# Optimization experiments

Measured on AMD Instinct MI355X. Metric: run time of the kernel, lower is better.

Reference implementation:

```python
import jax, jax.numpy as jnp
import numpy as np

N_NODES = 100000


def gcn_conv(x, src, dst, W, b):
    """PyG GCNConv: add self-loops, symmetric D^-1/2 (A+I) D^-1/2 normalization.
    x: [N, Fin]; src/dst: [E'] (self-loops already appended); W: [Fin, Fout]; b: [Fout].
    """
    xw = x @ W  # [N, Fout]
    ones = jnp.ones(dst.shape[0], dtype=x.dtype)
    deg = jax.ops.segment_sum(ones, dst, num_segments=N_NODES)  # in-degree incl. self-loop
    dinv = jnp.where(deg > 0, jax.lax.rsqrt(deg), 0.0)
    norm = dinv[src] * dinv[dst]  # [E']
    msg = xw[src] * norm[:, None]  # gather + scale
    out = jax.ops.segment_sum(msg, dst, num_segments=N_NODES)  # scatter-add
    return out + b


def setup_inputs() -> dict:
    key = jax.random.key(0)
    ks = jax.random.split(key, 12)
    hidden = 64
    E = 1600000
    x_node = jax.random.normal(ks[0], (N_NODES, 1), dtype=jnp.float32)
    edge_index = jax.random.randint(ks[1], (2, E), 0, N_NODES, dtype=jnp.int64)

    def glorot(k, fan_in, fan_out):
        lim = float(np.sqrt(6.0 / (fan_in + fan_out)))
        return jax.random.uniform(k, (fan_in, fan_out), jnp.float32, -lim, lim)

    W1 = glorot(ks[2], 1, hidden)
    b1 = jnp.zeros((hidden,), jnp.float32)
    W2 = glorot(ks[3], hidden, hidden)
    b2 = jnp.zeros((hidden,), jnp.float32)
    W3 = glorot(ks[4], hidden, hidden)
    b3 = jnp.zeros((hidden,), jnp.float32)
    W4 = glorot(ks[5], hidden, 1)
    b4 = jnp.zeros((1,), jnp.float32)
    return {"x_node": x_node, "edge_index": edge_index,
            "W1": W1, "b1": b1, "W2": W2, "b2": b2,
            "W3": W3, "b3": b3, "W4": W4, "b4": b4}


def reference(x_node, edge_index, W1, b1, W2, b2, W3, b3, W4, b4):
    # Append self-loops once (shared by both GCN layers, as PyG does per-layer with identical result)
    loops = jnp.arange(N_NODES, dtype=edge_index.dtype)
    src = jnp.concatenate([edge_index[0], loops])
    dst = jnp.concatenate([edge_index[1], loops])

    h = jax.nn.silu(gcn_conv(x_node, src, dst, W1, b1))
    h = jax.nn.silu(gcn_conv(h, src, dst, W2, b2))
    h = jax.nn.silu(h @ W3 + b3)
    return h @ W4 + b4  # [N, 1]
```

## Files before the change

### kernel.cpp

```cpp
#include <hip/hip_runtime.h>
#include <math.h>

#define N_NODES 100000
#define NPB    196
#define NBUCK  511
#define CAP    3584
#define CHUNKA 2048

#define NCHEB  15
#define SMAX   8.0f

__device__ __forceinline__ float silu_f(float x) {
    return x * __builtin_amdgcn_rcpf(1.0f + __builtin_amdgcn_exp2f(-1.442695041f * x));
}

__device__ __forceinline__ float bcast_f(float v, int lane) {
    return __int_as_float(__builtin_amdgcn_readlane(__float_as_int(v), lane));
}

__global__ __launch_bounds__(64) void k_cheb(const float* __restrict__ W1,
                                             const float* __restrict__ b1,
                                             float* __restrict__ cheb) {
    int f = threadIdx.x;
    float w = W1[f], b = b1[f];
    float g[NCHEB], th[NCHEB];
    const float pi = 3.14159265358979f;
#pragma unroll
    for (int j = 0; j < NCHEB; ++j) {
        th[j] = (j + 0.5f) * (pi / NCHEB);
        float S = SMAX * __cosf(th[j]);
        float y = fmaf(w, S, b);
        g[j] = y / (1.0f + expf(-y));
    }
#pragma unroll
    for (int k = 0; k < NCHEB; ++k) {
        float s = 0.f;
#pragma unroll
        for (int j = 0; j < NCHEB; ++j)
            s += g[j] * __cosf((float)k * th[j]);
        cheb[k * 64 + f] = s * ((k == 0) ? (1.0f / NCHEB) : (2.0f / NCHEB));
    }
}

__global__ __launch_bounds__(512) void k_bucket(const int* __restrict__ src,
                                                const int* __restrict__ dst,
                                                int* __restrict__ gcur,
                                                unsigned int* __restrict__ buf, int E) {
    __shared__ unsigned hist[512];
    __shared__ unsigned lbase[512];
    __shared__ unsigned gbase[512];
    __shared__ unsigned lcur[512];
    __shared__ unsigned wtot[8];
    __shared__ unsigned pay[CHUNKA];
    __shared__ unsigned short bkt[CHUNKA];
    int t = threadIdx.x;
    int lane = t & 63, wid = t >> 6;
    hist[t] = 0;
    __syncthreads();
    int e0 = blockIdx.x * CHUNKA;
    int e1 = min(e0 + CHUNKA, E);
    for (int e = e0 + t; e < e1; e += 512)
        atomicAdd(&hist[dst[e] / NPB], 1u);
    __syncthreads();
    unsigned v = hist[t], sc = v;
#pragma unroll
    for (int off = 1; off < 64; off <<= 1) {
        unsigned y = __shfl_up(sc, off, 64);
        if (lane >= off) sc += y;
    }
    if (lane == 63) wtot[wid] = sc;
    __syncthreads();
    unsigned add = 0;
    for (int w = 0; w < wid; ++w) add += wtot[w];
    unsigned ex = sc - v + add;
    lbase[t] = ex;
    gbase[t] = v ? (unsigned)atomicAdd(&gcur[t], (int)v) : 0u;
    lcur[t] = 0;
    __syncthreads();
    for (int e = e0 + t; e < e1; e += 512) {
        int d = dst[e];
        int s = src[e];
        int b = d / NPB;
        unsigned pos = lbase[b] + atomicAdd(&lcur[b], 1u);
        pay[pos] = ((unsigned)s << 8) | (unsigned)(d - b * NPB);
        bkt[pos] = (unsigned short)b;
    }
    __syncthreads();
    int cb = e1 - e0;
    for (int i = t; i < cb; i += 512) {
        int b = bkt[i];
        unsigned gp = gbase[b] + ((unsigned)i - lbase[b]);
        if (gp < CAP)
            buf[(size_t)b * CAP + gp] = pay[i];
    }
}

__global__ __launch_bounds__(512) void k_build(const int* __restrict__ gcur,
                                               unsigned int* __restrict__ buf,
                                               const float* __restrict__ x,
                                               int* __restrict__ rowptr,
                                               int* __restrict__ cnt,
                                               float* __restrict__ dinv,
                                               float* __restrict__ xs, int N) {
    __shared__ unsigned hist[256];
    __shared__ unsigned cur[256];
    __shared__ unsigned wtot[4];
    __shared__ unsigned lsrc[CAP];
    int b = blockIdx.x;
    int t = threadIdx.x;
    int lane = t & 63, wid = t >> 6;
    int cb = min(gcur[b], CAP);
    int n0 = b * NPB;
    int np = min(N - n0, NPB);
    unsigned int* bb = buf + (size_t)b * CAP;

    if (t < 256) hist[t] = 0;
    __syncthreads();
    for (int i = t; i < cb; i += 512) atomicAdd(&hist[bb[i] & 255u], 1u);
    __syncthreads();
    unsigned v = (t < 256) ? hist[t] : 0u, sc = v;
#pragma unroll
    for (int off = 1; off < 64; off <<= 1) {
        unsigned y = __shfl_up(sc, off, 64);
        if (lane >= off) sc += y;
    }
    if (lane == 63 && t < 256) wtot[wid] = sc;
    __syncthreads();
    unsigned add = 0;
    for (int w = 0; w < wid && w < 4; ++w) add += wtot[w];
    unsigned ex = sc - v + add;
    if (t < 256) cur[t] = ex;
    if (t < np) {
        int node = n0 + t;
        int deg = (int)v;
        cnt[node] = deg;
        rowptr[node] = b * CAP + (int)ex;
        float dv = rsqrtf((float)(deg + 1));
        dinv[node] = dv;
        xs[node] = x[node] * dv;
    }
    __syncthreads();
    for (int i = t; i < cb; i += 512) {
        unsigned p = bb[i];
        unsigned pos = atomicAdd(&cur[p & 255u], 1u);
        lsrc[pos] = p >> 8;
    }
    __syncthreads();
    for (int i = t; i < cb; i += 512) bb[i] = lsrc[i];
}

__global__ __launch_bounds__(256) void k_sd(const int* __restrict__ rowptr,
                                            const int* __restrict__ cnt,
                                            const int* __restrict__ csr,
                                            const float* __restrict__ xs,
                                            const float* __restrict__ dinv,
                                            float2* __restrict__ sd, int N) {
    int t = blockIdx.x * 256 + threadIdx.x;
    int i = t >> 3, sub = t & 7;
    if (i >= N) return;
    int start = rowptr[i], deg = cnt[i];
    float sum = 0.f;
    int ia = (sub < deg) ? csr[start + sub] : -1;
    int ib = (sub + 8 < deg) ? csr[start + sub + 8] : -1;
    if (ia >= 0) sum += xs[ia];
    if (ib >= 0) sum += xs[ib];
    for (int j = sub + 16; j < deg; j += 8) sum += xs[csr[start + j]];
    sum += __shfl_xor(sum, 1, 64);
    sum += __shfl_xor(sum, 2, 64);
    sum += __shfl_xor(sum, 4, 64);
    if (sub == 0) {
        float d = dinv[i];
        sd[i] = make_float2((sum + xs[i]) * d, d);
    }
}

__global__ __launch_bounds__(256, 8) void k_final(
    const int* __restrict__ rowptr, const int* __restrict__ cnt,
    const int* __restrict__ csr, const float2* __restrict__ sd,
    const float* __restrict__ cheb,
    const float* __restrict__ W2, const float* __restrict__ b2,
    const float* __restrict__ W3, const float* __restrict__ b3,
    const float* __restrict__ W4, const float* __restrict__ b4,
    float* __restrict__ out, int N)
{
    __shared__ float sA[64 * 65];
    __shared__ float sP[4 * 64];

    const int lane = threadIdx.x & 63;
    const int wid  = __builtin_amdgcn_readfirstlane(threadIdx.x >> 6);
    const int tile0 = blockIdx.x * 64;
    const int nbase = tile0 + wid * 16;
    const int row0  = wid * 16;

    const int nloc = lane >> 2, sub = lane & 3;
    const int i = nbase + nloc;
    const bool valid = (i < N);
    int start = 0, deg = 0;
    float2 self = make_float2(0.f, 0.f);
    if (valid) {
        start = rowptr[i];
        deg   = cnt[i];
        self  = sd[i];
    }

    float m[NCHEB];
    {
        float d = (sub == 0) ? self.y : 0.f;
        float t = fminf(fmaxf(self.x * (1.0f / SMAX), -1.f), 1.f);
        float t2 = t + t, Tm = 1.f, Tc = t;
        m[0] = d;
        m[1] = d * t;
#pragma unroll
        for (int k = 2; k < NCHEB; ++k) {
            float Tn = fmaf(t2, Tc, -Tm);
            m[k] = d * Tn;
            Tm = Tc; Tc = Tn;
        }
    }
    for (int j = sub; j < deg; j += 4) {
        int u = csr[start + j];
        float2 su = sd[u];
        float d = su.y;
        float t = fminf(fmaxf(su.x * (1.0f / SMAX), -1.f), 1.f);
        float t2 = t + t, Tm = 1.f, Tc = t;
        m[0] += d;
        m[1] = fmaf(d, t, m[1]);
#pragma unroll
        for (int k = 2; k < NCHEB; ++k) {
            float Tn = fmaf(t2, Tc, -Tm);
            m[k] = fmaf(d, Tn, m[k]);
            Tm = Tc; Tc = Tn;
        }
    }
#pragma unroll
    for (int k = 0; k < NCHEB; ++k) {
        m[k] += __shfl_xor(m[k], 1, 64);
        m[k] += __shfl_xor(m[k], 2, 64);
    }

    float ck[NCHEB];
#pragma unroll
    for (int k = 0; k < NCHEB; ++k) ck[k] = cheb[k * 64 + lane];
#pragma unroll
    for (int nl = 0; nl < 16; ++nl) {
        float acc = 0.f;
#pragma unroll
        for (int k = 0; k < NCHEB; ++k)
            acc = fmaf(ck[k], bcast_f(m[k], 4 * nl), acc);
        float dv = bcast_f(self.y, 4 * nl);
        sA[(row0 + nl) * 65 + lane] = acc * dv;
    }
    __syncthreads();

    const int f0 = wid * 16;
    float acc2[16];
#pragma unroll
    for (int j = 0; j < 16; ++j) acc2[j] = b2[f0 + j];
    for (int k = 0; k < 64; ++k) {
        float av = sA[lane * 65 + k];
#pragma unroll
        for (int j = 0; j < 16; ++j)
            acc2[j] = fmaf(av, W2[k * 64 + f0 + j], acc2[j]);
    }
    __syncthreads();
#pragma unroll
    for (int j = 0; j < 16; ++j)
        sA[lane * 65 + f0 + j] = silu_f(acc2[j]);
    __syncthreads();

    float acc3[16];
#pragma unroll
    for (int j = 0; j < 16; ++j) acc3[j] = b3[f0 + j];
    for (int k = 0; k < 64; ++k) {
        float uv = sA[lane * 65 + k];
#pragma unroll
        for (int j = 0; j < 16; ++j)
            acc3[j] = fmaf(uv, W3[k * 64 + f0 + j], acc3[j]);
    }
    float part = 0.f;
#pragma unroll
    for (int j = 0; j < 16; ++j)
        part = fmaf(silu_f(acc3[j]), W4[f0 + j], part);
    sP[wid * 64 + lane] = part;
    __syncthreads();

    if (wid == 0) {
        int i2 = tile0 + lane;
        if (i2 < N)
            out[i2] = sP[lane] + sP[64 + lane] + sP[128 + lane] + sP[192 + lane] + b4[0];
    }
}

extern "C" void kernel_launch(void* const* d_in, const int* in_sizes, int n_in,
                              void* d_out, int out_size, void* d_ws, size_t ws_size,
                              hipStream_t stream) {
    const float* x  = (const float*)d_in[0];
    const int* edge = (const int*)d_in[1];
    const float* W1 = (const float*)d_in[2];
    const float* b1 = (const float*)d_in[3];
    const float* W2 = (const float*)d_in[4];
    const float* b2 = (const float*)d_in[5];
    const float* W3 = (const float*)d_in[6];
    const float* b3 = (const float*)d_in[7];
    const float* W4 = (const float*)d_in[8];
    const float* b4 = (const float*)d_in[9];
    float* out = (float*)d_out;

    const int N = N_NODES;
    const int E = in_sizes[1] / 2;
    const int* src = edge;
    const int* dst = edge + E;
    const int NCHUNK = (E + CHUNKA - 1) / CHUNKA;

    char* ws = (char*)d_ws;
    size_t off = 0;
    int*    gcur   = (int*)(ws + off);    off += 512 * 4;
    float2* sd     = (float2*)(ws + off); off += (size_t)N * 8;
    int*    rowptr = (int*)(ws + off);    off += (size_t)N * 4;
    int*    cnt    = (int*)(ws + off);    off += (size_t)N * 4;
    float*  dinv   = (float*)(ws + off);  off += (size_t)N * 4;
    float*  xs     = (float*)(ws + off);  off += (size_t)N * 4;
    float*  cheb   = (float*)(ws + off);  off += NCHEB * 64 * 4;
    unsigned int* buf = (unsigned int*)(ws + off); off += (size_t)NBUCK * CAP * 4;
    int* csr = (int*)buf;

    hipMemsetAsync(gcur, 0, 512 * 4, stream);

    k_cheb  <<<1, 64, 0, stream>>>(W1, b1, cheb);
    k_bucket<<<NCHUNK, 512, 0, stream>>>(src, dst, gcur, buf, E);
    k_build <<<NBUCK, 512, 0, stream>>>(gcur, buf, x, rowptr, cnt, dinv, xs, N);
    k_sd    <<<(N * 8 + 255) / 256, 256, 0, stream>>>(rowptr, cnt, csr, xs, dinv, sd, N);
    k_final <<<(N + 63) / 64, 256, 0, stream>>>(rowptr, cnt, csr, sd, cheb,
                                                W2, b2, W3, b3, W4, b4, out, N);
}
```

Before: 165.8 us.

## Replace bucketed CSR build with atomic degree count, global scan and scatter

```diff
diff --git a/kernel.cpp b/kernel.cpp
--- a/kernel.cpp
+++ b/kernel.cpp
@@ -2,13 +2,9 @@
 #include <math.h>
 
 #define N_NODES 100000
-#define NPB    196
-#define NBUCK  511
-#define CAP    3584
-#define CHUNKA 2048
-
 #define NCHEB  15
 #define SMAX   8.0f
+#define SCAN_B 391
 
 __device__ __forceinline__ float silu_f(float x) {
     return x * __builtin_amdgcn_rcpf(1.0f + __builtin_amdgcn_exp2f(-1.442695041f * x));
@@ -18,159 +14,116 @@
     return __int_as_float(__builtin_amdgcn_readlane(__float_as_int(v), lane));
 }
 
-__global__ __launch_bounds__(64) void k_cheb(const float* __restrict__ W1,
+__global__ __launch_bounds__(256) void k_deg(const int* __restrict__ dst,
+                                             int* __restrict__ cnt,
+                                             const float* __restrict__ W1,
                                              const float* __restrict__ b1,
-                                             float* __restrict__ cheb) {
-    int f = threadIdx.x;
-    float w = W1[f], b = b1[f];
-    float g[NCHEB], th[NCHEB];
-    const float pi = 3.14159265358979f;
-#pragma unroll
-    for (int j = 0; j < NCHEB; ++j) {
-        th[j] = (j + 0.5f) * (pi / NCHEB);
-        float S = SMAX * __cosf(th[j]);
-        float y = fmaf(w, S, b);
-        g[j] = y / (1.0f + expf(-y));
-    }
-#pragma unroll
-    for (int k = 0; k < NCHEB; ++k) {
-        float s = 0.f;
-#pragma unroll
-        for (int j = 0; j < NCHEB; ++j)
-            s += g[j] * __cosf((float)k * th[j]);
-        cheb[k * 64 + f] = s * ((k == 0) ? (1.0f / NCHEB) : (2.0f / NCHEB));
-    }
-}
-
-__global__ __launch_bounds__(512) void k_bucket(const int* __restrict__ src,
-                                                const int* __restrict__ dst,
-                                                int* __restrict__ gcur,
-                                                unsigned int* __restrict__ buf, int E) {
-    __shared__ unsigned hist[512];
-    __shared__ unsigned lbase[512];
-    __shared__ unsigned gbase[512];
-    __shared__ unsigned lcur[512];
-    __shared__ unsigned wtot[8];
-    __shared__ unsigned pay[CHUNKA];
-    __shared__ unsigned short bkt[CHUNKA];
-    int t = threadIdx.x;
-    int lane = t & 63, wid = t >> 6;
-    hist[t] = 0;
-    __syncthreads();
-    int e0 = blockIdx.x * CHUNKA;
-    int e1 = min(e0 + CHUNKA, E);
-    for (int e = e0 + t; e < e1; e += 512)
-        atomicAdd(&hist[dst[e] / NPB], 1u);
-    __syncthreads();
-    unsigned v = hist[t], sc = v;
-#pragma unroll
-    for (int off = 1; off < 64; off <<= 1) {
-        unsigned y = __shfl_up(sc, off, 64);
-        if (lane >= off) sc += y;
-    }
-    if (lane == 63) wtot[wid] = sc;
-    __syncthreads();
-    unsigned add = 0;
-    for (int w = 0; w < wid; ++w) add += wtot[w];
-    unsigned ex = sc - v + add;
-    lbase[t] = ex;
-    gbase[t] = v ? (unsigned)atomicAdd(&gcur[t], (int)v) : 0u;
-    lcur[t] = 0;
-    __syncthreads();
-    for (int e = e0 + t; e < e1; e += 512) {
-        int d = dst[e];
-        int s = src[e];
-        int b = d / NPB;
-        unsigned pos = lbase[b] + atomicAdd(&lcur[b], 1u);
-        pay[pos] = ((unsigned)s << 8) | (unsigned)(d - b * NPB);
-        bkt[pos] = (unsigned short)b;
-    }
-    __syncthreads();
-    int cb = e1 - e0;
-    for (int i = t; i < cb; i += 512) {
-        int b = bkt[i];
-        unsigned gp = gbase[b] + ((unsigned)i - lbase[b]);
-        if (gp < CAP)
-            buf[(size_t)b * CAP + gp] = pay[i];
-    }
-}
-
-__global__ __launch_bounds__(512) void k_build(const int* __restrict__ gcur,
-                                               unsigned int* __restrict__ buf,
+                                             float* __restrict__ cheb, int E) {
+    int e = blockIdx.x * 256 + threadIdx.x;
+    if (e < E) atomicAdd(&cnt[dst[e]], 1);
+    if (blockIdx.x == 0 && threadIdx.x < 64) {
+        int f = threadIdx.x;
+        float w = W1[f], b = b1[f];
+        float g[NCHEB], th[NCHEB];
+        const float pi = 3.14159265358979f;
+#pragma unroll
+        for (int j = 0; j < NCHEB; ++j) {
+            th[j] = (j + 0.5f) * (pi / NCHEB);
+            float S = SMAX * __cosf(th[j]);
+            float y = fmaf(w, S, b);
+            g[j] = y / (1.0f + expf(-y));
+        }
+#pragma unroll
+        for (int k = 0; k < NCHEB; ++k) {
+            float s = 0.f;
+#pragma unroll
+            for (int j = 0; j < NCHEB; ++j)
+                s += g[j] * __cosf((float)k * th[j]);
+            cheb[k * 64 + f] = s * ((k == 0) ? (1.0f / NCHEB) : (2.0f / NCHEB));
+        }
+    }
+}
+
+__global__ __launch_bounds__(256) void k_scan1(const int* __restrict__ cnt,
+                                               int* __restrict__ bsum, int N) {
+    __shared__ unsigned wt[4];
+    int t = threadIdx.x, lane = t & 63, wid = t >> 6;
+    int i = blockIdx.x * 256 + t;
+    unsigned s = (i < N) ? (unsigned)cnt[i] : 0u;
+#pragma unroll
+    for (int o = 1; o < 64; o <<= 1) s += __shfl_xor(s, o, 64);
+    if (lane == 0) wt[wid] = s;
+    __syncthreads();
+    if (t == 0) bsum[blockIdx.x] = (int)(wt[0] + wt[1] + wt[2] + wt[3]);
+}
+
+__global__ __launch_bounds__(256) void k_scan2(const int* __restrict__ cnt,
+                                               const int* __restrict__ bsum,
                                                const float* __restrict__ x,
                                                int* __restrict__ rowptr,
-                                               int* __restrict__ cnt,
+                                               int* __restrict__ cur,
                                                float* __restrict__ dinv,
                                                float* __restrict__ xs, int N) {
-    __shared__ unsigned hist[256];
-    __shared__ unsigned cur[256];
-    __shared__ unsigned wtot[4];
-    __shared__ unsigned lsrc[CAP];
+    __shared__ unsigned wt[4];
+    int t = threadIdx.x, lane = t & 63, wid = t >> 6;
     int b = blockIdx.x;
-    int t = threadIdx.x;
-    int lane = t & 63, wid = t >> 6;
-    int cb = min(gcur[b], CAP);
-    int n0 = b * NPB;
-    int np = min(N - n0, NPB);
-    unsigned int* bb = buf + (size_t)b * CAP;
-
-    if (t < 256) hist[t] = 0;
-    __syncthreads();
-    for (int i = t; i < cb; i += 512) atomicAdd(&hist[bb[i] & 255u], 1u);
-    __syncthreads();
-    unsigned v = (t < 256) ? hist[t] : 0u, sc = v;
-#pragma unroll
-    for (int off = 1; off < 64; off <<= 1) {
-        unsigned y = __shfl_up(sc, off, 64);
-        if (lane >= off) sc += y;
-    }
-    if (lane == 63 && t < 256) wtot[wid] = sc;
+    int i = b * 256 + t;
+    unsigned v = (i < N) ? (unsigned)cnt[i] : 0u;
+
+    unsigned pp = 0;
+    if (t < b) pp = (unsigned)bsum[t];
+    if (t + 256 < b) pp += (unsigned)bsum[t + 256];
+    unsigned rs = pp;
+#pragma unroll
+    for (int o = 1; o < 64; o <<= 1) rs += __shfl_xor(rs, o, 64);
+    if (lane == 0) wt[wid] = rs;
+    __syncthreads();
+    unsigned boff = wt[0] + wt[1] + wt[2] + wt[3];
+    __syncthreads();
+
+    unsigned sc = v;
+#pragma unroll
+    for (int o = 1; o < 64; o <<= 1) {
+        unsigned y = __shfl_up(sc, o, 64);
+        if (lane >= o) sc += y;
+    }
+    if (lane == 63) wt[wid] = sc;
     __syncthreads();
     unsigned add = 0;
-    for (int w = 0; w < wid && w < 4; ++w) add += wtot[w];
-    unsigned ex = sc - v + add;
-    if (t < 256) cur[t] = ex;
-    if (t < np) {
-        int node = n0 + t;
-        int deg = (int)v;
-        cnt[node] = deg;
-        rowptr[node] = b * CAP + (int)ex;
-        float dv = rsqrtf((float)(deg + 1));
-        dinv[node] = dv;
-        xs[node] = x[node] * dv;
-    }
-    __syncthreads();
-    for (int i = t; i < cb; i += 512) {
-        unsigned p = bb[i];
-        unsigned pos = atomicAdd(&cur[p & 255u], 1u);
-        lsrc[pos] = p >> 8;
-    }
-    __syncthreads();
-    for (int i = t; i < cb; i += 512) bb[i] = lsrc[i];
-}
-
-__global__ __launch_bounds__(256) void k_sd(const int* __restrict__ rowptr,
-                                            const int* __restrict__ cnt,
-                                            const int* __restrict__ csr,
-                                            const float* __restrict__ xs,
-                                            const float* __restrict__ dinv,
-                                            float2* __restrict__ sd, int N) {
-    int t = blockIdx.x * 256 + threadIdx.x;
-    int i = t >> 3, sub = t & 7;
-    if (i >= N) return;
-    int start = rowptr[i], deg = cnt[i];
-    float sum = 0.f;
-    int ia = (sub < deg) ? csr[start + sub] : -1;
-    int ib = (sub + 8 < deg) ? csr[start + sub + 8] : -1;
-    if (ia >= 0) sum += xs[ia];
-    if (ib >= 0) sum += xs[ib];
-    for (int j = sub + 16; j < deg; j += 8) sum += xs[csr[start + j]];
-    sum += __shfl_xor(sum, 1, 64);
-    sum += __shfl_xor(sum, 2, 64);
-    sum += __shfl_xor(sum, 4, 64);
-    if (sub == 0) {
+    for (int w = 0; w < wid; ++w) add += wt[w];
+    unsigned ex = sc - v + add + boff;
+
+    if (i < N) {
+        rowptr[i] = (int)ex;
+        cur[i]    = (int)ex;
+        float dv = rsqrtf((float)(v + 1u));
+        dinv[i] = dv;
+        xs[i] = x[i] * dv;
+    }
+}
+
+__global__ __launch_bounds__(256) void k_scatter(const int* __restrict__ src,
+                                                 const int* __restrict__ dst,
+                                                 int* __restrict__ cur,
+                                                 int* __restrict__ csr,
+                                                 const float* __restrict__ xs,
+                                                 float* __restrict__ ssum, int E) {
+    int e = blockIdx.x * 256 + threadIdx.x;
+    if (e >= E) return;
+    int d = dst[e], s = src[e];
+    int p = atomicAdd(&cur[d], 1);
+    csr[p] = s;
+    atomicAdd(&ssum[d], xs[s]);
+}
+
+__global__ __launch_bounds__(256) void k_sd2(const float* __restrict__ ssum,
+                                             const float* __restrict__ xs,
+                                             const float* __restrict__ dinv,
+                                             float2* __restrict__ sd, int N) {
+    int i = blockIdx.x * 256 + threadIdx.x;
+    if (i < N) {
         float d = dinv[i];
-        sd[i] = make_float2((sum + xs[i]) * d, d);
+        sd[i] = make_float2((ssum[i] + xs[i]) * d, d);
     }
 }
 
@@ -310,26 +263,28 @@
     const int E = in_sizes[1] / 2;
     const int* src = edge;
     const int* dst = edge + E;
-    const int NCHUNK = (E + CHUNKA - 1) / CHUNKA;
+    const int EB = (E + 255) / 256;
 
     char* ws = (char*)d_ws;
     size_t off = 0;
-    int*    gcur   = (int*)(ws + off);    off += 512 * 4;
-    float2* sd     = (float2*)(ws + off); off += (size_t)N * 8;
+    int*    cnt    = (int*)(ws + off);    off += (size_t)N * 4;
+    float*  ssum   = (float*)(ws + off);  off += (size_t)N * 4;
     int*    rowptr = (int*)(ws + off);    off += (size_t)N * 4;
-    int*    cnt    = (int*)(ws + off);    off += (size_t)N * 4;
+    int*    cur    = (int*)(ws + off);    off += (size_t)N * 4;
     float*  dinv   = (float*)(ws + off);  off += (size_t)N * 4;
     float*  xs     = (float*)(ws + off);  off += (size_t)N * 4;
+    float2* sd     = (float2*)(ws + off); off += (size_t)N * 8;
     float*  cheb   = (float*)(ws + off);  off += NCHEB * 64 * 4;
-    unsigned int* buf = (unsigned int*)(ws + off); off += (size_t)NBUCK * CAP * 4;
-    int* csr = (int*)buf;
-
-    hipMemsetAsync(gcur, 0, 512 * 4, stream);
-
-    k_cheb  <<<1, 64, 0, stream>>>(W1, b1, cheb);
-    k_bucket<<<NCHUNK, 512, 0, stream>>>(src, dst, gcur, buf, E);
-    k_build <<<NBUCK, 512, 0, stream>>>(gcur, buf, x, rowptr, cnt, dinv, xs, N);
-    k_sd    <<<(N * 8 + 255) / 256, 256, 0, stream>>>(rowptr, cnt, csr, xs, dinv, sd, N);
-    k_final <<<(N + 63) / 64, 256, 0, stream>>>(rowptr, cnt, csr, sd, cheb,
-                                                W2, b2, W3, b3, W4, b4, out, N);
-}
+    int*    bsum   = (int*)(ws + off);    off += 512 * 4;
+    int*    csr    = (int*)(ws + off);    off += (size_t)E * 4;
+
+    hipMemsetAsync(cnt, 0, (size_t)2 * N * 4, stream);
+
+    k_deg    <<<EB, 256, 0, stream>>>(dst, cnt, W1, b1, cheb, E);
+    k_scan1  <<<SCAN_B, 256, 0, stream>>>(cnt, bsum, N);
+    k_scan2  <<<SCAN_B, 256, 0, stream>>>(cnt, bsum, x, rowptr, cur, dinv, xs, N);
+    k_scatter<<<EB, 256, 0, stream>>>(src, dst, cur, csr, xs, ssum, E);
+    k_sd2    <<<SCAN_B, 256, 0, stream>>>(ssum, xs, dinv, sd, N);
+    k_final  <<<(N + 63) / 64, 256, 0, stream>>>(rowptr, cnt, csr, sd, cheb,
+                                                 W2, b2, W3, b3, W4, b4, out, N);
+}
```

After: 350.2 us. 2.11x slower.
